# Performance work log

Hardware: AMD Instinct MI355X
Metric: run time of the kernel (lower is better)

## Reference

```python
import jax, jax.numpy as jnp
import numpy as np

# Config matching init_kwargs
B, C, H, W = 16, 256, 128, 128
RED, MID, NHEADS, G, WS = 64, 32, 4, 4, 8
SCALE = (MID // NHEADS) ** -0.5
EPS = 1e-5


def _bn(x, gamma, beta, mean, var):
    # eval-mode BatchNorm2d over channel dim of NCHW
    inv = gamma / jnp.sqrt(var + EPS)
    return x * inv[None, :, None, None] + (beta - mean * inv)[None, :, None, None]


def _gconv1d(x, w, b=None):
    # grouped 1x1 Conv1d: x (B, Cin, N), w (G, Cout_g, Cin_g)
    Bx, Cin, N = x.shape
    g, cout_g, cin_g = w.shape
    xg = x.reshape(Bx, g, cin_g, N)
    y = jnp.einsum('bgin,goi->bgon', xg, w).reshape(Bx, g * cout_g, N)
    if b is not None:
        y = y + b[None, :, None]
    return y


def setup_inputs() -> dict:
    key = jax.random.key(0)
    ks = jax.random.split(key, 20)
    s = 0.05
    d = {
        'x': jax.random.normal(ks[0], (B, C, H, W), jnp.float32),
        'bn_in_gamma': jnp.ones((C,), jnp.float32),
        'bn_in_beta': jnp.zeros((C,), jnp.float32),
        'bn_in_mean': jax.random.normal(ks[1], (C,), jnp.float32) * s,
        'bn_in_var': jax.random.uniform(ks[2], (C,), jnp.float32, 0.5, 1.5),
        'in_proj_w': jax.random.normal(ks[3], (RED, C), jnp.float32) * s,
        'qk_base_w': jax.random.normal(ks[4], (G, MID // G, RED // G), jnp.float32) * s,
        'q_head_w': jax.random.normal(ks[5], (MID, MID), jnp.float32) * s,
        'q_head_b': jnp.zeros((MID,), jnp.float32),
        'k_head_w': jax.random.normal(ks[6], (MID, MID), jnp.float32) * s,
        'k_head_b': jnp.zeros((MID,), jnp.float32),
        'v_w': jax.random.normal(ks[7], (G, MID // G, RED // G), jnp.float32) * s,
        'v_b': jnp.zeros((MID,), jnp.float32),
        'o_w': jax.random.normal(ks[8], (G, RED // G, MID // G), jnp.float32) * s,
        'o_b': jnp.zeros((RED,), jnp.float32),
        'out_proj_w': jax.random.normal(ks[9], (C, RED), jnp.float32) * s,
        'bn_out_gamma': jnp.ones((C,), jnp.float32),
        'bn_out_beta': jnp.zeros((C,), jnp.float32),
        'bn_out_mean': jax.random.normal(ks[10], (C,), jnp.float32) * s,
        'bn_out_var': jax.random.uniform(ks[11], (C,), jnp.float32, 0.5, 1.5),
        'alpha': jnp.zeros((), jnp.float32),
    }
    return d


def reference(x, bn_in_gamma, bn_in_beta, bn_in_mean, bn_in_var, in_proj_w,
              qk_base_w, q_head_w, q_head_b, k_head_w, k_head_b,
              v_w, v_b, o_w, o_b, out_proj_w,
              bn_out_gamma, bn_out_beta, bn_out_mean, bn_out_var, alpha):
    identity = x
    xn = _bn(x, bn_in_gamma, bn_in_beta, bn_in_mean, bn_in_var)
    x_red = jnp.einsum('oc,bchw->bohw', in_proj_w, xn)  # (B, RED, H, W)

    # window partition (H, W divisible by WS -> no padding)
    nH, nW = H // WS, W // WS
    xw = x_red.reshape(B, RED, nH, WS, nW, WS)
    xw = xw.transpose(0, 2, 4, 1, 3, 5).reshape(B * nH * nW, RED, WS * WS)

    # attention on N = WS*WS tokens per window
    base = _gconv1d(xw, qk_base_w)                              # (Bw, MID, N)
    q = jnp.einsum('oi,bin->bon', q_head_w, base) + q_head_b[None, :, None]
    k = jnp.einsum('oi,bin->bon', k_head_w, base) + k_head_b[None, :, None]
    v = _gconv1d(xw, v_w, v_b)

    def split_heads(t):
        Bw, Cm, N = t.shape
        return t.reshape(Bw, NHEADS, Cm // NHEADS, N).transpose(0, 1, 3, 2)  # (Bw,h,N,hd)

    q, k, v = split_heads(q), split_heads(k), split_heads(v)
    attn = jax.nn.softmax(jnp.einsum('bhnd,bhmd->bhnm', q, k) * SCALE, axis=-1)
    out = jnp.einsum('bhnm,bhmd->bhnd', attn, v)                # (Bw,h,N,hd)
    Bw = out.shape[0]
    out = out.transpose(0, 1, 3, 2).reshape(Bw, MID, WS * WS)
    out = _gconv1d(out, o_w, o_b)                               # (Bw, RED, N)

    # merge windows
    out = out.reshape(B, nH, nW, RED, WS, WS)
    out = out.transpose(0, 3, 1, 4, 2, 5).reshape(B, RED, H, W)

    out = jnp.einsum('oc,bchw->bohw', out_proj_w, out)          # (B, C, H, W)
    out = _bn(out, bn_out_gamma, bn_out_beta, bn_out_mean, bn_out_var)
    return identity + jax.nn.sigmoid(alpha) * out
```

## Files before the change

kernel.cpp:

```cpp
#include <hip/hip_runtime.h>
#include <math.h>

constexpr int Bb   = 16;
constexpr int Cc   = 256;
constexpr int Hh   = 128;
constexpr int Ww   = 128;
constexpr int NPIX = Hh * Ww;
constexpr int RED  = 64;
constexpr int MID  = 32;
constexpr float SCALE = 0.35355339059327373f;

__global__ __launch_bounds__(256) void prep_kernel(
    const float* __restrict__ bn_in_gamma, const float* __restrict__ bn_in_beta,
    const float* __restrict__ bn_in_mean,  const float* __restrict__ bn_in_var,
    const float* __restrict__ in_proj_w,
    const float* __restrict__ out_proj_w,
    const float* __restrict__ bn_out_gamma, const float* __restrict__ bn_out_beta,
    const float* __restrict__ bn_out_mean,  const float* __restrict__ bn_out_var,
    const float* __restrict__ o_w, const float* __restrict__ o_b,
    const float* __restrict__ alpha,
    float* __restrict__ WtIn,  float* __restrict__ beff_in,
    float* __restrict__ WtCmb, float* __restrict__ bcomb) {
  int idx = blockIdx.x * 256 + threadIdx.x;
  float s = 1.0f / (1.0f + __expf(-alpha[0]));
  if (idx < Cc * RED) {
    int c = idx >> 6, r = idx & 63;
    float inv = bn_in_gamma[c] * rsqrtf(bn_in_var[c] + 1e-5f);
    WtIn[idx] = in_proj_w[r * Cc + c] * inv;
  }
  if (idx < MID * Cc) {
    int m = idx >> 8, co = idx & 255;
    int g = m >> 3, j = m & 7;
    float inv2 = bn_out_gamma[co] * rsqrtf(bn_out_var[co] + 1e-5f);
    float a = 0.f;
    #pragma unroll
    for (int t = 0; t < 16; t++)
      a += out_proj_w[co * RED + g * 16 + t] * o_w[g * 128 + t * 8 + j];
    WtCmb[idx] = s * inv2 * a;
  }
  if (idx < RED) {
    float acc = 0.f;
    for (int c = 0; c < Cc; c++) {
      float inv = bn_in_gamma[c] * rsqrtf(bn_in_var[c] + 1e-5f);
      acc += in_proj_w[idx * Cc + c] * (bn_in_beta[c] - bn_in_mean[c] * inv);
    }
    beff_in[idx] = acc;
  }
  if (idx < Cc) {
    float inv2 = bn_out_gamma[idx] * rsqrtf(bn_out_var[idx] + 1e-5f);
    float a = bn_out_beta[idx] - bn_out_mean[idx] * inv2;
    for (int r = 0; r < RED; r++)
      a += inv2 * out_proj_w[idx * RED + r] * o_b[r];
    bcomb[idx] = s * a;
  }
}

__global__ __launch_bounds__(256, 3) void fused_kernel(
    const float* __restrict__ x,
    const float* __restrict__ WtIn,
    const float* __restrict__ beff_in,
    const float* __restrict__ qk_base_w, const float* __restrict__ q_head_w,
    const float* __restrict__ q_head_b,  const float* __restrict__ k_head_w,
    const float* __restrict__ k_head_b,  const float* __restrict__ v_w,
    const float* __restrict__ v_b,
    const float* __restrict__ WtCmb,
    const float* __restrict__ bcomb,
    float* __restrict__ out) {
  __shared__ float smem[13440];
  float* XR    = smem;
  float* base_ = smem + 4096;
  float* kT    = smem + 6144;
  float* vT    = smem + 8256;
  float* qkw   = smem + 10368;
  float* vw    = smem + 10880;
  float* qhw   = smem + 11392;
  float* khw   = smem + 12416;
  float* Xc    = smem + 4096;
  float* outT  = base_;

  const int bid = blockIdx.x;
  const int w   = ((bid & 7) << 9) | (bid >> 3);
  const int b   = w >> 8;
  const int wh  = (w >> 4) & 15, wwi = w & 15;
  const int tid  = threadIdx.x;
  const int lane = tid & 63;
  const int wv   = __builtin_amdgcn_readfirstlane(tid >> 6);

  const float* xwin = x + ((size_t)b * Cc) * NPIX + (wh * 8) * Ww + wwi * 8;

  float acc[16];
  #pragma unroll
  for (int t = 0; t < 16; t++) acc[t] = beff_in[wv * 16 + t];
  for (int ch = 0; ch < 4; ch++) {
    __syncthreads();
    for (int e = tid; e < 1024; e += 256) {
      int cc = e >> 4, nq = e & 15;
      int i = nq >> 1, half = nq & 1;
      float4 xv4 = *(const float4*)(xwin + (size_t)(ch * 64 + cc) * NPIX + i * Ww + half * 4);
      *(float4*)(Xc + cc * 64 + nq * 4) = xv4;
    }
    __syncthreads();
    const float* Wp = WtIn + (size_t)(ch * 64) * 64 + wv * 16;
    #pragma unroll
    for (int k = 0; k < 64; k++) {
      float xv = Xc[k * 64 + lane];
      const float* wk = Wp + k * 64;
      #pragma unroll
      for (int t = 0; t < 16; t++) acc[t] = fmaf(wk[t], xv, acc[t]);
    }
  }
  #pragma unroll
  for (int t = 0; t < 16; t++) XR[(wv * 16 + t) * 64 + lane] = acc[t];
  for (int e = tid; e < 512; e += 256)  { qkw[e] = qk_base_w[e]; vw[e] = v_w[e]; }
  for (int e = tid; e < 1024; e += 256) { qhw[e] = q_head_w[e]; khw[e] = k_head_w[e]; }
  __syncthreads();

  for (int e = tid; e < 2048; e += 256) {
    int m = e >> 6, n = e & 63, g = m >> 3;
    const float* wp = qkw + (g * 8 + (m & 7)) * 16;
    const float* xp = XR + g * 16 * 64 + n;
    float a = 0.f;
    #pragma unroll
    for (int i = 0; i < 16; i++) a += wp[i] * xp[i * 64];
    base_[e] = a;
  }
  __syncthreads();

  for (int e = tid; e < 2048; e += 256) {
    int m = e >> 6, n = e & 63, g = m >> 3;
    float a = k_head_b[m];
    const float* wp = khw + m * 32;
    #pragma unroll
    for (int i = 0; i < 32; i++) a += wp[i] * base_[i * 64 + n];
    kT[n * 33 + m] = a;
    float av = v_b[m];
    const float* vp = vw + (g * 8 + (m & 7)) * 16;
    const float* xp = XR + g * 16 * 64 + n;
    #pragma unroll
    for (int i = 0; i < 16; i++) av += vp[i] * xp[i * 64];
    vT[n * 33 + m] = av;
  }
  __syncthreads();

  float qv[8];
  {
    float a[8];
    #pragma unroll
    for (int d = 0; d < 8; d++) a[d] = q_head_b[wv * 8 + d];
    #pragma unroll
    for (int i = 0; i < 32; i++) {
      float bv = base_[i * 64 + lane];
      #pragma unroll
      for (int d = 0; d < 8; d++) a[d] += qhw[(wv * 8 + d) * 32 + i] * bv;
    }
    #pragma unroll
    for (int d = 0; d < 8; d++) qv[d] = a[d] * SCALE;
  }
  float s[64];
  float mx = -1e30f;
  const float* kTh = kT + wv * 8;
  #pragma unroll
  for (int j = 0; j < 64; j++) {
    const float* kr = kTh + j * 33;
    float a = 0.f;
    #pragma unroll
    for (int d = 0; d < 8; d++) a += qv[d] * kr[d];
    s[j] = a;
    mx = fmaxf(mx, a);
  }
  float sum = 0.f;
  #pragma unroll
  for (int j = 0; j < 64; j++) { float e = __expf(s[j] - mx); s[j] = e; sum += e; }
  float inv = 1.0f / sum;
  float o[8] = {0, 0, 0, 0, 0, 0, 0, 0};
  const float* vTh = vT + wv * 8;
  #pragma unroll
  for (int j = 0; j < 64; j++) {
    float p = s[j];
    const float* vr = vTh + j * 33;
    #pragma unroll
    for (int d = 0; d < 8; d++) o[d] += p * vr[d];
  }
  __syncthreads();
  #pragma unroll
  for (int d = 0; d < 8; d++) outT[(wv * 8 + d) * 64 + lane] = o[d] * inv;
  __syncthreads();

  const int ii = lane >> 3, jj = lane & 7;
  const size_t pixoff = (size_t)(wh * 8 + ii) * Ww + wwi * 8 + jj;
  for (int cc = 0; cc < 4; cc++) {
    const int co0 = cc * 64 + wv * 16;
    float oacc[16];
    #pragma unroll
    for (int t = 0; t < 16; t++) oacc[t] = bcomb[co0 + t];
    const float* Wp = WtCmb + co0;
    #pragma unroll
    for (int k = 0; k < 32; k++) {
      float yv = outT[k * 64 + lane];
      const float* wk = Wp + k * 256;
      #pragma unroll
      for (int t = 0; t < 16; t++) oacc[t] = fmaf(wk[t], yv, oacc[t]);
    }
    const float* xr = x   + ((size_t)b * Cc + co0) * NPIX + pixoff;
    float*       orr = out + ((size_t)b * Cc + co0) * NPIX + pixoff;
    #pragma unroll
    for (int t = 0; t < 16; t++) {
      orr[(size_t)t * NPIX] = oacc[t] + xr[(size_t)t * NPIX];
    }
  }
}

extern "C" void kernel_launch(void* const* d_in, const int* in_sizes, int n_in,
                              void* d_out, int out_size, void* d_ws, size_t ws_size,
                              hipStream_t stream) {
  const float* x           = (const float*)d_in[0];
  const float* bn_in_gamma = (const float*)d_in[1];
  const float* bn_in_beta  = (const float*)d_in[2];
  const float* bn_in_mean  = (const float*)d_in[3];
  const float* bn_in_var   = (const float*)d_in[4];
  const float* in_proj_w   = (const float*)d_in[5];
  const float* qk_base_w   = (const float*)d_in[6];
  const float* q_head_w    = (const float*)d_in[7];
  const float* q_head_b    = (const float*)d_in[8];
  const float* k_head_w    = (const float*)d_in[9];
  const float* k_head_b    = (const float*)d_in[10];
  const float* v_w         = (const float*)d_in[11];
  const float* v_b         = (const float*)d_in[12];
  const float* o_w         = (const float*)d_in[13];
  const float* o_b         = (const float*)d_in[14];
  const float* out_proj_w  = (const float*)d_in[15];
  const float* bn_out_gamma= (const float*)d_in[16];
  const float* bn_out_beta = (const float*)d_in[17];
  const float* bn_out_mean = (const float*)d_in[18];
  const float* bn_out_var  = (const float*)d_in[19];
  const float* alpha       = (const float*)d_in[20];

  float* ws = (float*)d_ws;
  float* WtIn    = ws;
  float* beff_in = ws + 16384;
  float* WtCmb   = ws + 16448;
  float* bcomb   = ws + 24640;
  (void)ws_size; (void)in_sizes; (void)n_in; (void)out_size;

  prep_kernel<<<64, 256, 0, stream>>>(
      bn_in_gamma, bn_in_beta, bn_in_mean, bn_in_var, in_proj_w,
      out_proj_w, bn_out_gamma, bn_out_beta, bn_out_mean, bn_out_var,
      o_w, o_b, alpha, WtIn, beff_in, WtCmb, bcomb);

  fused_kernel<<<4096, 256, 0, stream>>>(
      x, WtIn, beff_in, qk_base_w, q_head_w, q_head_b, k_head_w, k_head_b,
      v_w, v_b, WtCmb, bcomb, (float*)d_out);
}
```

Baseline: 777.7 us.

## Restructure attention stage into per-thread registers, shrink LDS, prefetch input chunks

Each thread now computes base, q, k and v for its own pixel in registers, reading the small weights directly from global/constant memory instead of staging them in LDS. This removes two barriers and the LDS weight copies, and shrinks shared memory from about 53KB to 35KB so occupancy can rise from 3 to 4 blocks per CU. It also adds register double-buffered prefetch of the next input channel chunk, uses padded float4 LDS rows for K/V, and caches the attention output in registers for the final projection. The risk is higher register pressure (base_[32], yv[32], s_[64]) under the tighter launch bound, which could cause spills.

```diff
diff --git a/kernel.cpp b/kernel.cpp
--- a/kernel.cpp
+++ b/kernel.cpp
@@ -55,7 +55,7 @@
   }
 }
 
-__global__ __launch_bounds__(256, 3) void fused_kernel(
+__global__ __launch_bounds__(256, 4) void fused_kernel(
     const float* __restrict__ x,
     const float* __restrict__ WtIn,
     const float* __restrict__ beff_in,
@@ -66,17 +66,12 @@
     const float* __restrict__ WtCmb,
     const float* __restrict__ bcomb,
     float* __restrict__ out) {
-  __shared__ float smem[13440];
-  float* XR    = smem;
-  float* base_ = smem + 4096;
-  float* kT    = smem + 6144;
-  float* vT    = smem + 8256;
-  float* qkw   = smem + 10368;
-  float* vw    = smem + 10880;
-  float* qhw   = smem + 11392;
-  float* khw   = smem + 12416;
-  float* Xc    = smem + 4096;
-  float* outT  = base_;
+  __shared__ float smem[8704];
+  float* kT   = smem;
+  float* vT   = smem + 2304;
+  float* Xc   = smem;
+  float* XR   = smem + 4608;
+  float* outT = smem + 4608;
 
   const int bid = blockIdx.x;
   const int w   = ((bid & 7) << 9) | (bid >> 3);
@@ -91,13 +86,25 @@
   float acc[16];
   #pragma unroll
   for (int t = 0; t < 16; t++) acc[t] = beff_in[wv * 16 + t];
+
+  const int s_cc = tid >> 4, s_nq = tid & 15;
+  const size_t s_goff = (size_t)s_cc * NPIX + (s_nq >> 1) * Ww + (s_nq & 1) * 4;
+
+  float4 pre[4];
+  #pragma unroll
+  for (int i = 0; i < 4; i++)
+    pre[i] = *(const float4*)(xwin + (size_t)(0 * 64 + i * 16) * NPIX + s_goff);
+
+  #pragma unroll
   for (int ch = 0; ch < 4; ch++) {
     __syncthreads();
-    for (int e = tid; e < 1024; e += 256) {
-      int cc = e >> 4, nq = e & 15;
-      int i = nq >> 1, half = nq & 1;
-      float4 xv4 = *(const float4*)(xwin + (size_t)(ch * 64 + cc) * NPIX + i * Ww + half * 4);
-      *(float4*)(Xc + cc * 64 + nq * 4) = xv4;
+    #pragma unroll
+    for (int i = 0; i < 4; i++)
+      *(float4*)(Xc + (s_cc + i * 16) * 64 + s_nq * 4) = pre[i];
+    if (ch < 3) {
+      #pragma unroll
+      for (int i = 0; i < 4; i++)
+        pre[i] = *(const float4*)(xwin + (size_t)((ch + 1) * 64 + i * 16) * NPIX + s_goff);
     }
     __syncthreads();
     const float* Wp = WtIn + (size_t)(ch * 64) * 64 + wv * 16;
@@ -111,81 +118,95 @@
   }
   #pragma unroll
   for (int t = 0; t < 16; t++) XR[(wv * 16 + t) * 64 + lane] = acc[t];
-  for (int e = tid; e < 512; e += 256)  { qkw[e] = qk_base_w[e]; vw[e] = v_w[e]; }
-  for (int e = tid; e < 1024; e += 256) { qhw[e] = q_head_w[e]; khw[e] = k_head_w[e]; }
   __syncthreads();
 
-  for (int e = tid; e < 2048; e += 256) {
-    int m = e >> 6, n = e & 63, g = m >> 3;
-    const float* wp = qkw + (g * 8 + (m & 7)) * 16;
-    const float* xp = XR + g * 16 * 64 + n;
-    float a = 0.f;
-    #pragma unroll
-    for (int i = 0; i < 16; i++) a += wp[i] * xp[i * 64];
-    base_[e] = a;
-  }
+  float base_[32];
+  #pragma unroll
+  for (int g = 0; g < 4; g++) {
+    float xr[16];
+    #pragma unroll
+    for (int t = 0; t < 16; t++) xr[t] = XR[(g * 16 + t) * 64 + lane];
+    #pragma unroll
+    for (int o = 0; o < 8; o++) {
+      const float* wp = qk_base_w + (g * 8 + o) * 16;
+      float a = 0.f;
+      #pragma unroll
+      for (int t = 0; t < 16; t++) a += wp[t] * xr[t];
+      base_[g * 8 + o] = a;
+    }
+  }
+  float vacc[8];
+  {
+    float xr[16];
+    #pragma unroll
+    for (int t = 0; t < 16; t++) xr[t] = XR[(wv * 16 + t) * 64 + lane];
+    #pragma unroll
+    for (int d = 0; d < 8; d++) {
+      const float* vp = v_w + (wv * 8 + d) * 16;
+      float a = v_b[wv * 8 + d];
+      #pragma unroll
+      for (int t = 0; t < 16; t++) a += vp[t] * xr[t];
+      vacc[d] = a;
+    }
+  }
+  float qv[8];
+  #pragma unroll
+  for (int d = 0; d < 8; d++) {
+    const float* wp = q_head_w + (wv * 8 + d) * 32;
+    float a = q_head_b[wv * 8 + d];
+    #pragma unroll
+    for (int i = 0; i < 32; i++) a += wp[i] * base_[i];
+    qv[d] = a * SCALE;
+  }
+  float kacc[8];
+  #pragma unroll
+  for (int d = 0; d < 8; d++) {
+    const float* wp = k_head_w + (wv * 8 + d) * 32;
+    float a = k_head_b[wv * 8 + d];
+    #pragma unroll
+    for (int i = 0; i < 32; i++) a += wp[i] * base_[i];
+    kacc[d] = a;
+  }
+  *(float4*)(kT + lane * 36 + wv * 8)     = make_float4(kacc[0], kacc[1], kacc[2], kacc[3]);
+  *(float4*)(kT + lane * 36 + wv * 8 + 4) = make_float4(kacc[4], kacc[5], kacc[6], kacc[7]);
+  *(float4*)(vT + lane * 36 + wv * 8)     = make_float4(vacc[0], vacc[1], vacc[2], vacc[3]);
+  *(float4*)(vT + lane * 36 + wv * 8 + 4) = make_float4(vacc[4], vacc[5], vacc[6], vacc[7]);
   __syncthreads();
 
-  for (int e = tid; e < 2048; e += 256) {
-    int m = e >> 6, n = e & 63, g = m >> 3;
-    float a = k_head_b[m];
-    const float* wp = khw + m * 32;
-    #pragma unroll
-    for (int i = 0; i < 32; i++) a += wp[i] * base_[i * 64 + n];
-    kT[n * 33 + m] = a;
-    float av = v_b[m];
-    const float* vp = vw + (g * 8 + (m & 7)) * 16;
-    const float* xp = XR + g * 16 * 64 + n;
-    #pragma unroll
-    for (int i = 0; i < 16; i++) av += vp[i] * xp[i * 64];
-    vT[n * 33 + m] = av;
-  }
-  __syncthreads();
-
-  float qv[8];
-  {
-    float a[8];
-    #pragma unroll
-    for (int d = 0; d < 8; d++) a[d] = q_head_b[wv * 8 + d];
-    #pragma unroll
-    for (int i = 0; i < 32; i++) {
-      float bv = base_[i * 64 + lane];
-      #pragma unroll
-      for (int d = 0; d < 8; d++) a[d] += qhw[(wv * 8 + d) * 32 + i] * bv;
-    }
-    #pragma unroll
-    for (int d = 0; d < 8; d++) qv[d] = a[d] * SCALE;
-  }
-  float s[64];
+  float s_[64];
   float mx = -1e30f;
   const float* kTh = kT + wv * 8;
   #pragma unroll
   for (int j = 0; j < 64; j++) {
-    const float* kr = kTh + j * 33;
+    float4 k0 = *(const float4*)(kTh + j * 36);
+    float4 k1 = *(const float4*)(kTh + j * 36 + 4);
     float a = 0.f;
-    #pragma unroll
-    for (int d = 0; d < 8; d++) a += qv[d] * kr[d];
-    s[j] = a;
+    a += qv[0] * k0.x; a += qv[1] * k0.y; a += qv[2] * k0.z; a += qv[3] * k0.w;
+    a += qv[4] * k1.x; a += qv[5] * k1.y; a += qv[6] * k1.z; a += qv[7] * k1.w;
+    s_[j] = a;
     mx = fmaxf(mx, a);
   }
   float sum = 0.f;
   #pragma unroll
-  for (int j = 0; j < 64; j++) { float e = __expf(s[j] - mx); s[j] = e; sum += e; }
+  for (int j = 0; j < 64; j++) { float e = __expf(s_[j] - mx); s_[j] = e; sum += e; }
   float inv = 1.0f / sum;
   float o[8] = {0, 0, 0, 0, 0, 0, 0, 0};
   const float* vTh = vT + wv * 8;
   #pragma unroll
   for (int j = 0; j < 64; j++) {
-    float p = s[j];
-    const float* vr = vTh + j * 33;
-    #pragma unroll
-    for (int d = 0; d < 8; d++) o[d] += p * vr[d];
-  }
-  __syncthreads();
+    float p = s_[j];
+    float4 v0 = *(const float4*)(vTh + j * 36);
+    float4 v1 = *(const float4*)(vTh + j * 36 + 4);
+    o[0] += p * v0.x; o[1] += p * v0.y; o[2] += p * v0.z; o[3] += p * v0.w;
+    o[4] += p * v1.x; o[5] += p * v1.y; o[6] += p * v1.z; o[7] += p * v1.w;
+  }
   #pragma unroll
   for (int d = 0; d < 8; d++) outT[(wv * 8 + d) * 64 + lane] = o[d] * inv;
   __syncthreads();
 
+  float yv[32];
+  #pragma unroll
+  for (int k = 0; k < 32; k++) yv[k] = outT[k * 64 + lane];
   const int ii = lane >> 3, jj = lane & 7;
   const size_t pixoff = (size_t)(wh * 8 + ii) * Ww + wwi * 8 + jj;
   for (int cc = 0; cc < 4; cc++) {
@@ -196,17 +217,16 @@
     const float* Wp = WtCmb + co0;
     #pragma unroll
     for (int k = 0; k < 32; k++) {
-      float yv = outT[k * 64 + lane];
+      float y = yv[k];
       const float* wk = Wp + k * 256;
       #pragma unroll
-      for (int t = 0; t < 16; t++) oacc[t] = fmaf(wk[t], yv, oacc[t]);
-    }
-    const float* xr = x   + ((size_t)b * Cc + co0) * NPIX + pixoff;
+      for (int t = 0; t < 16; t++) oacc[t] = fmaf(wk[t], y, oacc[t]);
+    }
+    const float* xr  = x   + ((size_t)b * Cc + co0) * NPIX + pixoff;
     float*       orr = out + ((size_t)b * Cc + co0) * NPIX + pixoff;
     #pragma unroll
-    for (int t = 0; t < 16; t++) {
+    for (int t = 0; t < 16; t++)
       orr[(size_t)t * NPIX] = oacc[t] + xr[(size_t)t * NPIX];
-    }
   }
 }
 
```

Result: no change. 765.9 us (-1.5%).
